# Kernel tuning notes

Hardware: AMD Instinct MI355X
Metric: run time of the kernel (lower is better)

Reference implementation:

```python
import jax, jax.numpy as jnp
import numpy as np

L = 32768          # sequence length (keys/values)
E = 1024           # embed_dim (hardcoded in module via weight slices)
H, D = 8, 128      # num_heads, head_dim (hardcoded via reshape(-1, 8, 128))


def setup_inputs() -> dict:
    key = jax.random.key(0)
    k1, k2, k3, k4, k5 = jax.random.split(key, 5)
    scale = 1.0 / np.sqrt(E)
    return {
        "x": jax.random.normal(k1, (L, E), dtype=jnp.float32),
        "in_proj_weight": jax.random.normal(k2, (3 * E, E), dtype=jnp.float32) * scale,
        "in_proj_bias": jax.random.normal(k3, (3 * E,), dtype=jnp.float32) * 0.02,
        "out_proj_weight": jax.random.normal(k4, (E, E), dtype=jnp.float32) * scale,
        "out_proj_bias": jax.random.normal(k5, (E,), dtype=jnp.float32) * 0.02,
    }


def reference(x, in_proj_weight, in_proj_bias, out_proj_weight, out_proj_bias):
    # Single-query (decode-style) attention: q from first token only.
    q = x[:1] @ in_proj_weight[:E].T + in_proj_bias[:E]              # [1, E]
    k = x @ in_proj_weight[E:2 * E].T + in_proj_bias[E:2 * E]        # [L, E]
    v = x @ in_proj_weight[2 * E:].T + in_proj_bias[2 * E:]          # [L, E]

    q = q.reshape(-1, H, D).transpose(1, 0, 2)                       # [H, 1, D]
    k = k.reshape(-1, H, D).transpose(1, 2, 0)                       # [H, D, L]
    v = v.reshape(-1, H, D).transpose(1, 0, 2)                       # [H, L, D]

    dot = jnp.matmul(q, k) * (1.0 / np.sqrt(D))                      # [H, 1, L]
    attn = jax.nn.softmax(dot, axis=-1)
    out = jnp.matmul(attn, v)                                        # [H, 1, D]

    out = out.transpose(1, 0, 2).reshape(-1, E)                      # [1, E]
    out = out @ out_proj_weight.T + out_proj_bias                    # [1, E]
    return out
```

## Files before the change

kernel.cpp:

```cpp
#include <hip/hip_runtime.h>
#include <math.h>


#define L_SEQ   32768
#define E_DIM   1024
#define NHEAD   8
#define HDIM    128
#define TILE_R  8
#define WAVES_M 8

#define GLD16(gp, lp)                                                   \
  __builtin_amdgcn_global_load_lds(                                     \
      (const __attribute__((address_space(1))) void*)(gp),              \
      (__attribute__((address_space(3))) void*)(lp), 16, 0, 0)

__global__ __launch_bounds__(256) void proj_q(
    const float* __restrict__ W, const float* __restrict__ bias,
    const float* __restrict__ x, float* __restrict__ q)
{
  const int t = threadIdx.x, wave = t >> 6, lane = t & 63;
  const int o = blockIdx.x * 4 + wave;
  const float4* Wr = (const float4*)(W + (size_t)o * E_DIM);
  const float4* xr = (const float4*)x;
  float a = 0.f;
#pragma unroll
  for (int k = 0; k < 4; ++k) {
    float4 wv = Wr[lane + 64 * k];
    float4 xv = xr[lane + 64 * k];
    a += wv.x * xv.x + wv.y * xv.y + wv.z * xv.z + wv.w * xv.w;
  }
#pragma unroll
  for (int m = 1; m < 64; m <<= 1) a += __shfl_xor(a, m, 64);
  if (lane == 0) q[o] = a + bias[o];
}

__global__ __launch_bounds__(256) void make_p(
    const float* __restrict__ W, const float* __restrict__ q,
    float* __restrict__ P_T)
{
  __shared__ __align__(16) float4 ps[8][32];
  const int t  = threadIdx.x;
  const int h  = blockIdx.y;
  const int ec = blockIdx.x;
  const int eg = t & 31;
  const int dg = t >> 5;
  const float* Wb = W + ((size_t)E_DIM + h * HDIM + dg * 16) * E_DIM + ec * 128 + eg * 4;
  const float* qh = q + h * HDIM + dg * 16;
  float4 a = make_float4(0.f, 0.f, 0.f, 0.f);
#pragma unroll
  for (int dd = 0; dd < 16; ++dd) {
    const float qv = qh[dd];
    const float4 wv = *(const float4*)(Wb + (size_t)dd * E_DIM);
    a.x += qv * wv.x; a.y += qv * wv.y; a.z += qv * wv.z; a.w += qv * wv.w;
  }
  ps[dg][eg] = a;
  __syncthreads();
  if (t < 32) {
    float4 s = ps[0][t];
#pragma unroll
    for (int g = 1; g < 8; ++g) {
      const float4 b = ps[g][t];
      s.x += b.x; s.y += b.y; s.z += b.z; s.w += b.w;
    }
    const float sc = 0.08838834764831845f;
    s.x *= sc; s.y *= sc; s.z *= sc; s.w *= sc;
    *(float4*)(P_T + (size_t)h * E_DIM + ec * 128 + t * 4) = s;
  }
}

__global__ __launch_bounds__(512, 2) void attn_fused5(
    const float* __restrict__ x,
    const float* __restrict__ P_T,
    float* __restrict__ partial_z,
    float* __restrict__ partial_sumw,
    int rows_per_blk)
{
  __shared__ __align__(16) float sbuf[2][TILE_R][E_DIM];
  __shared__ float swst[16];

  const int t    = threadIdx.x;
  const int wave = t >> 6;
  const int lane = t & 63;
  const int rh   = wave >> 2;
  const int h0   = (wave & 3) * 2;
  const size_t row0 = (size_t)blockIdx.x * rows_per_blk;
  const int ntiles  = rows_per_blk / TILE_R;

  float4 p0[4], p1[4];
  {
    const float4* P0 = (const float4*)(P_T + (size_t)h0 * E_DIM);
    const float4* P1 = (const float4*)(P_T + (size_t)(h0 + 1) * E_DIM);
#pragma unroll
    for (int k = 0; k < 4; ++k) { p0[k] = P0[64 * k + lane]; p1[k] = P1[64 * k + lane]; }
  }

  float4 z0[4], z1[4];
#pragma unroll
  for (int k = 0; k < 4; ++k) {
    z0[k] = make_float4(0.f, 0.f, 0.f, 0.f);
    z1[k] = make_float4(0.f, 0.f, 0.f, 0.f);
  }
  float sumw0 = 0.f, sumw1 = 0.f;

  {
    const float* g = x + (row0 + wave) * E_DIM + 4 * lane;
#pragma unroll
    for (int k = 0; k < 4; ++k) GLD16(g + k * 256, &sbuf[0][wave][k * 256]);
  }
  __syncthreads();

  for (int tile = 0; tile < ntiles; ++tile) {
    const int buf = tile & 1;

    if (tile + 1 < ntiles) {
      const float* g = x + (row0 + (size_t)(tile + 1) * TILE_R + wave) * E_DIM + 4 * lane;
#pragma unroll
      for (int k = 0; k < 4; ++k) GLD16(g + k * 256, &sbuf[buf ^ 1][wave][k * 256]);
    }

#pragma unroll
    for (int rl = 0; rl < 4; ++rl) {
      const float4* xr4 = (const float4*)&sbuf[buf][rh * 4 + rl][0];
      float4 xr[4];
#pragma unroll
      for (int k = 0; k < 4; ++k) xr[k] = xr4[64 * k + lane];

      float s0 = 0.f, s1 = 0.f;
#pragma unroll
      for (int k = 0; k < 4; ++k) {
        s0 += xr[k].x * p0[k].x + xr[k].y * p0[k].y + xr[k].z * p0[k].z + xr[k].w * p0[k].w;
        s1 += xr[k].x * p1[k].x + xr[k].y * p1[k].y + xr[k].z * p1[k].z + xr[k].w * p1[k].w;
      }

      const bool odd = (lane & 1);
      float keep = odd ? s1 : s0;
      float oth  = odd ? s0 : s1;
      float ts = keep + __shfl_xor(oth, 1, 64);
      ts += __shfl_xor(ts, 2, 64);
      ts += __shfl_xor(ts, 4, 64);
      ts += __shfl_xor(ts, 8, 64);
      ts += __shfl_xor(ts, 16, 64);
      ts += __shfl_xor(ts, 32, 64);
      const float ex = __expf(ts);
      const float ox = __shfl_xor(ex, 1, 64);
      const float w0 = odd ? ox : ex;
      const float w1 = odd ? ex : ox;
      sumw0 += w0; sumw1 += w1;

#pragma unroll
      for (int k = 0; k < 4; ++k) {
        z0[k].x += w0 * xr[k].x; z0[k].y += w0 * xr[k].y;
        z0[k].z += w0 * xr[k].z; z0[k].w += w0 * xr[k].w;
        z1[k].x += w1 * xr[k].x; z1[k].y += w1 * xr[k].y;
        z1[k].z += w1 * xr[k].z; z1[k].w += w1 * xr[k].w;
      }
    }

    __syncthreads();
  }

  float (*zs)[E_DIM] = (float(*)[E_DIM])&sbuf[0][0][0];
  {
    float4* zd0 = (float4*)&zs[2 * wave][0];
    float4* zd1 = (float4*)&zs[2 * wave + 1][0];
#pragma unroll
    for (int k = 0; k < 4; ++k) { zd0[64 * k + lane] = z0[k]; zd1[64 * k + lane] = z1[k]; }
  }
  if (lane == 0) { swst[2 * wave] = sumw0; swst[2 * wave + 1] = sumw1; }
  __syncthreads();

  {
    const float4* zsv = (const float4*)&zs[0][0];
    float4* pzb = (float4*)(partial_z + (size_t)blockIdx.x * (NHEAD * E_DIM));
#pragma unroll
    for (int j = 0; j < 4; ++j) {
      const int idx = t + 512 * j;
      const float4 a = zsv[idx], b = zsv[idx + 2048];
      pzb[idx] = make_float4(a.x + b.x, a.y + b.y, a.z + b.z, a.w + b.w);
    }
  }
  if (t < NHEAD)
    partial_sumw[blockIdx.x * NHEAD + t] = swst[t] + swst[t + 8];
}

__global__ __launch_bounds__(256) void reduce_z(
    const float* __restrict__ partial_z,
    const float* __restrict__ partial_sumw,
    float* __restrict__ zn, int nblk)
{
  __shared__ float red[256];
  __shared__ __align__(16) float swst[4][NHEAD];
  __shared__ float sumw_s[NHEAD];
  const int t = threadIdx.x;
  const int lane = t & 63, wave = t >> 6;

  float sw[NHEAD];
#pragma unroll
  for (int h = 0; h < NHEAD; ++h) sw[h] = 0.f;
  for (int b = t; b < nblk; b += 256) {
    const float4* p = (const float4*)(partial_sumw + (size_t)b * NHEAD);
    float4 a0 = p[0], a1 = p[1];
    sw[0] += a0.x; sw[1] += a0.y; sw[2] += a0.z; sw[3] += a0.w;
    sw[4] += a1.x; sw[5] += a1.y; sw[6] += a1.z; sw[7] += a1.w;
  }
#pragma unroll
  for (int m = 1; m < 64; m <<= 1) {
#pragma unroll
    for (int h = 0; h < NHEAD; ++h) sw[h] += __shfl_xor(sw[h], m, 64);
  }
  if (lane == 0) {
#pragma unroll
    for (int h = 0; h < NHEAD; ++h) swst[wave][h] = sw[h];
  }
  __syncthreads();
  if (t < NHEAD) sumw_s[t] = swst[0][t] + swst[1][t] + swst[2][t] + swst[3][t];

  const int o = blockIdx.x * 32 + (t & 31);
  const int g = t >> 5;
  float a = 0.f;
  for (int b = g; b < nblk; b += 8) a += partial_z[(size_t)b * (NHEAD * E_DIM) + o];
  red[t] = a;
  __syncthreads();
  if (t < 32) {
    float s2 = 0.f;
#pragma unroll
    for (int gg = 0; gg < 8; ++gg) s2 += red[gg * 32 + t];
    const int oo = blockIdx.x * 32 + t;
    zn[oo] = s2 / sumw_s[oo >> 10];
  }
}

__global__ __launch_bounds__(256) void proj_v(
    const float* __restrict__ W, const float* __restrict__ bias,
    const float* __restrict__ zn, float* __restrict__ attn)
{
  const int t = threadIdx.x, wave = t >> 6, lane = t & 63;
  const int o = blockIdx.x * 4 + wave;
  const float4* Wr = (const float4*)(W + ((size_t)2 * E_DIM + o) * E_DIM);
  const float4* zr = (const float4*)(zn + (size_t)(o >> 7) * E_DIM);
  float a = 0.f;
#pragma unroll
  for (int k = 0; k < 4; ++k) {
    float4 wv = Wr[lane + 64 * k];
    float4 zv = zr[lane + 64 * k];
    a += wv.x * zv.x + wv.y * zv.y + wv.z * zv.z + wv.w * zv.w;
  }
#pragma unroll
  for (int m = 1; m < 64; m <<= 1) a += __shfl_xor(a, m, 64);
  if (lane == 0) attn[o] = a + bias[2 * E_DIM + o];
}

__global__ __launch_bounds__(256) void proj_o(
    const float* __restrict__ Wo, const float* __restrict__ bo,
    const float* __restrict__ attn, float* __restrict__ out)
{
  const int t = threadIdx.x, wave = t >> 6, lane = t & 63;
  const int o = blockIdx.x * 4 + wave;
  const float4* Wr = (const float4*)(Wo + (size_t)o * E_DIM);
  const float4* vr = (const float4*)attn;
  float a = 0.f;
#pragma unroll
  for (int k = 0; k < 4; ++k) {
    float4 wv = Wr[lane + 64 * k];
    float4 vv = vr[lane + 64 * k];
    a += wv.x * vv.x + wv.y * vv.y + wv.z * vv.z + wv.w * vv.w;
  }
#pragma unroll
  for (int m = 1; m < 64; m <<= 1) a += __shfl_xor(a, m, 64);
  if (lane == 0) out[o] = a + bo[o];
}

extern "C" void kernel_launch(void* const* d_in, const int* in_sizes, int n_in,
                              void* d_out, int out_size, void* d_ws, size_t ws_size,
                              hipStream_t stream)
{
  const float* x  = (const float*)d_in[0];
  const float* Wi = (const float*)d_in[1];
  const float* bi = (const float*)d_in[2];
  const float* Wo = (const float*)d_in[3];
  const float* bo = (const float*)d_in[4];
  float* out = (float*)d_out;

  char* ws = (char*)d_ws;
  float* q     = (float*)(ws + 0);
  float* P_T   = (float*)(ws + 4096);
  float* zn    = (float*)(ws + 36864);
  float* attn  = (float*)(ws + 69632);
  float* psumw = (float*)(ws + 73728);
  const size_t pz_off = 90112;
  float* pz    = (float*)(ws + pz_off);

  int nblk = 128;
  if (ws_size >= pz_off + (size_t)512 * NHEAD * E_DIM * 4) nblk = 512;
  else if (ws_size >= pz_off + (size_t)256 * NHEAD * E_DIM * 4) nblk = 256;
  const int rows_per_blk = L_SEQ / nblk;

  proj_q     <<<256, 256, 0, stream>>>(Wi, bi, x, q);
  make_p     <<<dim3(8, 8), 256, 0, stream>>>(Wi, q, P_T);
  attn_fused5<<<nblk, 512, 0, stream>>>(x, P_T, pz, psumw, rows_per_blk);
  reduce_z   <<<256, 256, 0, stream>>>(pz, psumw, zn, nblk);
  proj_v     <<<256, 256, 0, stream>>>(Wi, bi, zn, attn);
  proj_o     <<<256, 256, 0, stream>>>(Wo, bo, attn, out);
}
```

Before: 242.6 us.

## Fuse all stages into one persistent kernel with software grid barriers

Replaces the six-kernel launch sequence with a single persistent kernel of 256 blocks that runs q projection, P construction, attention streaming, reduction and both output projections. Stages are separated by an atomic-counter grid barrier, so there is one launch instead of six and no inter-kernel gaps. In exchange, the attention stage uses 256 blocks instead of possibly 512, and the barrier depends on all blocks being co-resident, which could deadlock if they are not. A memset of the barrier is also added each call, and the fallback make_p path is rewritten to use one thread per output.

```diff
diff --git a/kernel.cpp b/kernel.cpp
--- a/kernel.cpp
+++ b/kernel.cpp
@@ -7,12 +7,278 @@
 #define NHEAD   8
 #define HDIM    128
 #define TILE_R  8
-#define WAVES_M 8
+#define NBLK    256
 
 #define GLD16(gp, lp)                                                   \
   __builtin_amdgcn_global_load_lds(                                     \
       (const __attribute__((address_space(1))) void*)(gp),              \
       (__attribute__((address_space(3))) void*)(lp), 16, 0, 0)
+
+__device__ __forceinline__ void grid_barrier(int* bar, int phase)
+{
+  __syncthreads();
+  if (threadIdx.x == 0) {
+    if (__hip_atomic_fetch_add(&bar[0], 1, __ATOMIC_ACQ_REL,
+                               __HIP_MEMORY_SCOPE_AGENT) == NBLK - 1) {
+      __hip_atomic_store(&bar[0], 0, __ATOMIC_RELAXED, __HIP_MEMORY_SCOPE_AGENT);
+      __hip_atomic_store(&bar[1], phase, __ATOMIC_RELEASE, __HIP_MEMORY_SCOPE_AGENT);
+    } else {
+      while (__hip_atomic_load(&bar[1], __ATOMIC_ACQUIRE,
+                               __HIP_MEMORY_SCOPE_AGENT) < phase) {}
+    }
+  }
+  __syncthreads();
+}
+
+__global__ __launch_bounds__(512, 2) void mha_all(
+    const float* __restrict__ x,   const float* __restrict__ Wi,
+    const float* __restrict__ bi,  const float* __restrict__ Wo,
+    const float* __restrict__ bo,  float* __restrict__ out,
+    float* __restrict__ q,   float* __restrict__ P_T,
+    float* __restrict__ zn,  float* __restrict__ attn,
+    float* __restrict__ psumw, float* __restrict__ pz,
+    int* bar)
+{
+  __shared__ __align__(16) float sbuf[2][TILE_R][E_DIM];
+  __shared__ float swst[16];
+  __shared__ __align__(16) float swst4[8][NHEAD];
+  __shared__ float sumw_s[NHEAD];
+
+  const int t    = threadIdx.x;
+  const int wave = t >> 6;
+  const int lane = t & 63;
+  const int bid  = blockIdx.x;
+
+  if (bid < 128) {
+    const int o = bid * 8 + wave;
+    const float4* Wr = (const float4*)(Wi + (size_t)o * E_DIM);
+    const float4* xr = (const float4*)x;
+    float a = 0.f;
+#pragma unroll
+    for (int k = 0; k < 4; ++k) {
+      float4 wv = Wr[lane + 64 * k];
+      float4 xv = xr[lane + 64 * k];
+      a += wv.x * xv.x + wv.y * xv.y + wv.z * xv.z + wv.w * xv.w;
+    }
+#pragma unroll
+    for (int m = 1; m < 64; m <<= 1) a += __shfl_xor(a, m, 64);
+    if (lane == 0) q[o] = a + bi[o];
+  }
+  grid_barrier(bar, 1);
+
+  if (bid < 128) {
+    float4 (*ps)[16] = (float4(*)[16])&sbuf[0][0][0];
+    const int h   = bid >> 4;
+    const int ec2 = bid & 15;
+    const int eg  = t & 15;
+    const int dg  = t >> 4;
+    const float* Wb = Wi + ((size_t)E_DIM + h * HDIM + dg * 4) * E_DIM + ec2 * 64 + eg * 4;
+    const float* qh = q + h * HDIM + dg * 4;
+    float4 a = make_float4(0.f, 0.f, 0.f, 0.f);
+#pragma unroll
+    for (int dd = 0; dd < 4; ++dd) {
+      const float qv = qh[dd];
+      const float4 wv = *(const float4*)(Wb + (size_t)dd * E_DIM);
+      a.x += qv * wv.x; a.y += qv * wv.y; a.z += qv * wv.z; a.w += qv * wv.w;
+    }
+    ps[dg][eg] = a;
+    __syncthreads();
+    if (t < 16) {
+      float4 s = ps[0][t];
+#pragma unroll
+      for (int g = 1; g < 32; ++g) {
+        const float4 b = ps[g][t];
+        s.x += b.x; s.y += b.y; s.z += b.z; s.w += b.w;
+      }
+      const float sc = 0.08838834764831845f;
+      s.x *= sc; s.y *= sc; s.z *= sc; s.w *= sc;
+      *(float4*)(P_T + (size_t)h * E_DIM + ec2 * 64 + t * 4) = s;
+    }
+  }
+  grid_barrier(bar, 2);
+
+  {
+    const int rh = wave >> 2;
+    const int h0 = (wave & 3) * 2;
+    const size_t row0 = (size_t)bid * (L_SEQ / NBLK);
+    const int ntiles  = (L_SEQ / NBLK) / TILE_R;
+
+    float4 p0[4], p1[4];
+    {
+      const float4* P0 = (const float4*)(P_T + (size_t)h0 * E_DIM);
+      const float4* P1 = (const float4*)(P_T + (size_t)(h0 + 1) * E_DIM);
+#pragma unroll
+      for (int k = 0; k < 4; ++k) { p0[k] = P0[64 * k + lane]; p1[k] = P1[64 * k + lane]; }
+    }
+
+    float4 z0[4], z1[4];
+#pragma unroll
+    for (int k = 0; k < 4; ++k) {
+      z0[k] = make_float4(0.f, 0.f, 0.f, 0.f);
+      z1[k] = make_float4(0.f, 0.f, 0.f, 0.f);
+    }
+    float sumw0 = 0.f, sumw1 = 0.f;
+
+    {
+      const float* g = x + (row0 + wave) * E_DIM + 4 * lane;
+#pragma unroll
+      for (int k = 0; k < 4; ++k) GLD16(g + k * 256, &sbuf[0][wave][k * 256]);
+    }
+    __syncthreads();
+
+    for (int tile = 0; tile < ntiles; ++tile) {
+      const int buf = tile & 1;
+
+      if (tile + 1 < ntiles) {
+        const float* g = x + (row0 + (size_t)(tile + 1) * TILE_R + wave) * E_DIM + 4 * lane;
+#pragma unroll
+        for (int k = 0; k < 4; ++k) GLD16(g + k * 256, &sbuf[buf ^ 1][wave][k * 256]);
+      }
+
+#pragma unroll
+      for (int rl = 0; rl < 4; ++rl) {
+        const float4* xr4 = (const float4*)&sbuf[buf][rh * 4 + rl][0];
+        float4 xr[4];
+#pragma unroll
+        for (int k = 0; k < 4; ++k) xr[k] = xr4[64 * k + lane];
+
+        float s0 = 0.f, s1 = 0.f;
+#pragma unroll
+        for (int k = 0; k < 4; ++k) {
+          s0 += xr[k].x * p0[k].x + xr[k].y * p0[k].y + xr[k].z * p0[k].z + xr[k].w * p0[k].w;
+          s1 += xr[k].x * p1[k].x + xr[k].y * p1[k].y + xr[k].z * p1[k].z + xr[k].w * p1[k].w;
+        }
+
+        const bool odd = (lane & 1);
+        float keep = odd ? s1 : s0;
+        float oth  = odd ? s0 : s1;
+        float ts = keep + __shfl_xor(oth, 1, 64);
+        ts += __shfl_xor(ts, 2, 64);
+        ts += __shfl_xor(ts, 4, 64);
+        ts += __shfl_xor(ts, 8, 64);
+        ts += __shfl_xor(ts, 16, 64);
+        ts += __shfl_xor(ts, 32, 64);
+        const float ex = __expf(ts);
+        const float ox = __shfl_xor(ex, 1, 64);
+        const float w0 = odd ? ox : ex;
+        const float w1 = odd ? ex : ox;
+        sumw0 += w0; sumw1 += w1;
+
+#pragma unroll
+        for (int k = 0; k < 4; ++k) {
+          z0[k].x += w0 * xr[k].x; z0[k].y += w0 * xr[k].y;
+          z0[k].z += w0 * xr[k].z; z0[k].w += w0 * xr[k].w;
+          z1[k].x += w1 * xr[k].x; z1[k].y += w1 * xr[k].y;
+          z1[k].z += w1 * xr[k].z; z1[k].w += w1 * xr[k].w;
+        }
+      }
+
+      __syncthreads();
+    }
+
+    float (*zs)[E_DIM] = (float(*)[E_DIM])&sbuf[0][0][0];
+    {
+      float4* zd0 = (float4*)&zs[2 * wave][0];
+      float4* zd1 = (float4*)&zs[2 * wave + 1][0];
+#pragma unroll
+      for (int k = 0; k < 4; ++k) { zd0[64 * k + lane] = z0[k]; zd1[64 * k + lane] = z1[k]; }
+    }
+    if (lane == 0) { swst[2 * wave] = sumw0; swst[2 * wave + 1] = sumw1; }
+    __syncthreads();
+
+    {
+      const float4* zsv = (const float4*)&zs[0][0];
+      float4* pzb = (float4*)(pz + (size_t)bid * (NHEAD * E_DIM));
+#pragma unroll
+      for (int j = 0; j < 4; ++j) {
+        const int idx = t + 512 * j;
+        const float4 a = zsv[idx], b = zsv[idx + 2048];
+        pzb[idx] = make_float4(a.x + b.x, a.y + b.y, a.z + b.z, a.w + b.w);
+      }
+    }
+    if (t < NHEAD)
+      psumw[bid * NHEAD + t] = swst[t] + swst[t + 8];
+  }
+  grid_barrier(bar, 3);
+
+  {
+    float* red = &sbuf[0][0][0];
+    float sw[NHEAD];
+#pragma unroll
+    for (int h = 0; h < NHEAD; ++h) sw[h] = 0.f;
+    for (int b2 = t; b2 < NBLK; b2 += 512) {
+      const float4* p = (const float4*)(psumw + (size_t)b2 * NHEAD);
+      float4 a0 = p[0], a1 = p[1];
+      sw[0] += a0.x; sw[1] += a0.y; sw[2] += a0.z; sw[3] += a0.w;
+      sw[4] += a1.x; sw[5] += a1.y; sw[6] += a1.z; sw[7] += a1.w;
+    }
+#pragma unroll
+    for (int m = 1; m < 64; m <<= 1) {
+#pragma unroll
+      for (int h = 0; h < NHEAD; ++h) sw[h] += __shfl_xor(sw[h], m, 64);
+    }
+    if (lane == 0) {
+#pragma unroll
+      for (int h = 0; h < NHEAD; ++h) swst4[wave][h] = sw[h];
+    }
+    __syncthreads();
+    if (t < NHEAD) {
+      float s = 0.f;
+#pragma unroll
+      for (int wv = 0; wv < 8; ++wv) s += swst4[wv][t];
+      sumw_s[t] = s;
+    }
+
+    const int o = bid * 32 + (t & 31);
+    const int g = t >> 5;
+    float a = 0.f;
+    for (int b2 = g; b2 < NBLK; b2 += 16) a += pz[(size_t)b2 * (NHEAD * E_DIM) + o];
+    red[t] = a;
+    __syncthreads();
+    if (t < 32) {
+      float s2 = 0.f;
+#pragma unroll
+      for (int gg = 0; gg < 16; ++gg) s2 += red[gg * 32 + t];
+      const int oo = bid * 32 + t;
+      zn[oo] = s2 / sumw_s[oo >> 10];
+    }
+  }
+  grid_barrier(bar, 4);
+
+  if (bid < 128) {
+    const int o = bid * 8 + wave;
+    const float4* Wr = (const float4*)(Wi + ((size_t)2 * E_DIM + o) * E_DIM);
+    const float4* zr = (const float4*)(zn + (size_t)(o >> 7) * E_DIM);
+    float a = 0.f;
+#pragma unroll
+    for (int k = 0; k < 4; ++k) {
+      float4 wv = Wr[lane + 64 * k];
+      float4 zv = zr[lane + 64 * k];
+      a += wv.x * zv.x + wv.y * zv.y + wv.z * zv.z + wv.w * zv.w;
+    }
+#pragma unroll
+    for (int m = 1; m < 64; m <<= 1) a += __shfl_xor(a, m, 64);
+    if (lane == 0) attn[o] = a + bi[2 * E_DIM + o];
+  }
+  grid_barrier(bar, 5);
+
+  if (bid < 128) {
+    const int o = bid * 8 + wave;
+    const float4* Wr = (const float4*)(Wo + (size_t)o * E_DIM);
+    const float4* vr = (const float4*)attn;
+    float a = 0.f;
+#pragma unroll
+    for (int k = 0; k < 4; ++k) {
+      float4 wv = Wr[lane + 64 * k];
+      float4 vv = vr[lane + 64 * k];
+      a += wv.x * vv.x + wv.y * vv.y + wv.z * vv.z + wv.w * vv.w;
+    }
+#pragma unroll
+    for (int m = 1; m < 64; m <<= 1) a += __shfl_xor(a, m, 64);
+    if (lane == 0) out[o] = a + bo[o];
+  }
+}
+
 
 __global__ __launch_bounds__(256) void proj_q(
     const float* __restrict__ W, const float* __restrict__ bias,
@@ -34,57 +300,36 @@
   if (lane == 0) q[o] = a + bias[o];
 }
 
-__global__ __launch_bounds__(256) void make_p(
+__global__ __launch_bounds__(128) void make_p(
     const float* __restrict__ W, const float* __restrict__ q,
     float* __restrict__ P_T)
 {
-  __shared__ __align__(16) float4 ps[8][32];
-  const int t  = threadIdx.x;
-  const int h  = blockIdx.y;
-  const int ec = blockIdx.x;
-  const int eg = t & 31;
-  const int dg = t >> 5;
-  const float* Wb = W + ((size_t)E_DIM + h * HDIM + dg * 16) * E_DIM + ec * 128 + eg * 4;
-  const float* qh = q + h * HDIM + dg * 16;
-  float4 a = make_float4(0.f, 0.f, 0.f, 0.f);
-#pragma unroll
-  for (int dd = 0; dd < 16; ++dd) {
-    const float qv = qh[dd];
-    const float4 wv = *(const float4*)(Wb + (size_t)dd * E_DIM);
-    a.x += qv * wv.x; a.y += qv * wv.y; a.z += qv * wv.z; a.w += qv * wv.w;
-  }
-  ps[dg][eg] = a;
-  __syncthreads();
-  if (t < 32) {
-    float4 s = ps[0][t];
-#pragma unroll
-    for (int g = 1; g < 8; ++g) {
-      const float4 b = ps[g][t];
-      s.x += b.x; s.y += b.y; s.z += b.z; s.w += b.w;
-    }
-    const float sc = 0.08838834764831845f;
-    s.x *= sc; s.y *= sc; s.z *= sc; s.w *= sc;
-    *(float4*)(P_T + (size_t)h * E_DIM + ec * 128 + t * 4) = s;
-  }
+  const int h = blockIdx.y;
+  const int e = blockIdx.x * 128 + threadIdx.x;
+  const float* qh = q + h * HDIM;
+  const float* Wb = W + ((size_t)E_DIM + (size_t)h * HDIM) * E_DIM + e;
+  float a0 = 0.f, a1 = 0.f, a2 = 0.f, a3 = 0.f;
+#pragma unroll 4
+  for (int d = 0; d < HDIM; d += 4) {
+    a0 += qh[d + 0] * Wb[(size_t)(d + 0) * E_DIM];
+    a1 += qh[d + 1] * Wb[(size_t)(d + 1) * E_DIM];
+    a2 += qh[d + 2] * Wb[(size_t)(d + 2) * E_DIM];
+    a3 += qh[d + 3] * Wb[(size_t)(d + 3) * E_DIM];
+  }
+  P_T[h * E_DIM + e] = ((a0 + a1) + (a2 + a3)) * 0.08838834764831845f;
 }
 
 __global__ __launch_bounds__(512, 2) void attn_fused5(
-    const float* __restrict__ x,
-    const float* __restrict__ P_T,
-    float* __restrict__ partial_z,
-    float* __restrict__ partial_sumw,
+    const float* __restrict__ x, const float* __restrict__ P_T,
+    float* __restrict__ partial_z, float* __restrict__ partial_sumw,
     int rows_per_blk)
 {
   __shared__ __align__(16) float sbuf[2][TILE_R][E_DIM];
   __shared__ float swst[16];
-
-  const int t    = threadIdx.x;
-  const int wave = t >> 6;
-  const int lane = t & 63;
-  const int rh   = wave >> 2;
-  const int h0   = (wave & 3) * 2;
+  const int t = threadIdx.x, wave = t >> 6, lane = t & 63;
+  const int rh = wave >> 2, h0 = (wave & 3) * 2;
   const size_t row0 = (size_t)blockIdx.x * rows_per_blk;
-  const int ntiles  = rows_per_blk / TILE_R;
+  const int ntiles = rows_per_blk / TILE_R;
 
   float4 p0[4], p1[4];
   {
@@ -93,7 +338,6 @@
 #pragma unroll
     for (int k = 0; k < 4; ++k) { p0[k] = P0[64 * k + lane]; p1[k] = P1[64 * k + lane]; }
   }
-
   float4 z0[4], z1[4];
 #pragma unroll
   for (int k = 0; k < 4; ++k) {
@@ -101,37 +345,31 @@
     z1[k] = make_float4(0.f, 0.f, 0.f, 0.f);
   }
   float sumw0 = 0.f, sumw1 = 0.f;
-
   {
     const float* g = x + (row0 + wave) * E_DIM + 4 * lane;
 #pragma unroll
     for (int k = 0; k < 4; ++k) GLD16(g + k * 256, &sbuf[0][wave][k * 256]);
   }
   __syncthreads();
-
   for (int tile = 0; tile < ntiles; ++tile) {
     const int buf = tile & 1;
-
     if (tile + 1 < ntiles) {
       const float* g = x + (row0 + (size_t)(tile + 1) * TILE_R + wave) * E_DIM + 4 * lane;
 #pragma unroll
       for (int k = 0; k < 4; ++k) GLD16(g + k * 256, &sbuf[buf ^ 1][wave][k * 256]);
     }
-
 #pragma unroll
     for (int rl = 0; rl < 4; ++rl) {
       const float4* xr4 = (const float4*)&sbuf[buf][rh * 4 + rl][0];
       float4 xr[4];
 #pragma unroll
       for (int k = 0; k < 4; ++k) xr[k] = xr4[64 * k + lane];
-
       float s0 = 0.f, s1 = 0.f;
 #pragma unroll
       for (int k = 0; k < 4; ++k) {
         s0 += xr[k].x * p0[k].x + xr[k].y * p0[k].y + xr[k].z * p0[k].z + xr[k].w * p0[k].w;
         s1 += xr[k].x * p1[k].x + xr[k].y * p1[k].y + xr[k].z * p1[k].z + xr[k].w * p1[k].w;
       }
-
       const bool odd = (lane & 1);
       float keep = odd ? s1 : s0;
       float oth  = odd ? s0 : s1;
@@ -146,7 +384,6 @@
       const float w0 = odd ? ox : ex;
       const float w1 = odd ? ex : ox;
       sumw0 += w0; sumw1 += w1;
-
 #pragma unroll
       for (int k = 0; k < 4; ++k) {
         z0[k].x += w0 * xr[k].x; z0[k].y += w0 * xr[k].y;
@@ -155,10 +392,8 @@
         z1[k].z += w1 * xr[k].z; z1[k].w += w1 * xr[k].w;
       }
     }
-
     __syncthreads();
   }
-
   float (*zs)[E_DIM] = (float(*)[E_DIM])&sbuf[0][0][0];
   {
     float4* zd0 = (float4*)&zs[2 * wave][0];
@@ -168,7 +403,6 @@
   }
   if (lane == 0) { swst[2 * wave] = sumw0; swst[2 * wave + 1] = sumw1; }
   __syncthreads();
-
   {
     const float4* zsv = (const float4*)&zs[0][0];
     float4* pzb = (float4*)(partial_z + (size_t)blockIdx.x * (NHEAD * E_DIM));
@@ -184,8 +418,7 @@
 }
 
 __global__ __launch_bounds__(256) void reduce_z(
-    const float* __restrict__ partial_z,
-    const float* __restrict__ partial_sumw,
+    const float* __restrict__ partial_z, const float* __restrict__ partial_sumw,
     float* __restrict__ zn, int nblk)
 {
   __shared__ float red[256];
@@ -193,7 +426,6 @@
   __shared__ float sumw_s[NHEAD];
   const int t = threadIdx.x;
   const int lane = t & 63, wave = t >> 6;
-
   float sw[NHEAD];
 #pragma unroll
   for (int h = 0; h < NHEAD; ++h) sw[h] = 0.f;
@@ -214,7 +446,6 @@
   }
   __syncthreads();
   if (t < NHEAD) sumw_s[t] = swst[0][t] + swst[1][t] + swst[2][t] + swst[3][t];
-
   const int o = blockIdx.x * 32 + (t & 31);
   const int g = t >> 5;
   float a = 0.f;
@@ -287,8 +518,17 @@
   float* zn    = (float*)(ws + 36864);
   float* attn  = (float*)(ws + 69632);
   float* psumw = (float*)(ws + 73728);
+  int*   bar   = (int*)  (ws + 81920);
   const size_t pz_off = 90112;
   float* pz    = (float*)(ws + pz_off);
+
+  const size_t need_coop = pz_off + (size_t)NBLK * NHEAD * E_DIM * 4;
+  if (ws_size >= need_coop) {
+    hipMemsetAsync(bar, 0, 64, stream);
+    mha_all<<<NBLK, 512, 0, stream>>>(x, Wi, bi, Wo, bo, out,
+                                      q, P_T, zn, attn, psumw, pz, bar);
+    return;
+  }
 
   int nblk = 128;
   if (ws_size >= pz_off + (size_t)512 * NHEAD * E_DIM * 4) nblk = 512;
@@ -296,7 +536,7 @@
   const int rows_per_blk = L_SEQ / nblk;
 
   proj_q     <<<256, 256, 0, stream>>>(Wi, bi, x, q);
-  make_p     <<<dim3(8, 8), 256, 0, stream>>>(Wi, q, P_T);
+  make_p     <<<dim3(8, 8), 128, 0, stream>>>(Wi, q, P_T);
   attn_fused5<<<nblk, 512, 0, stream>>>(x, P_T, pz, psumw, rows_per_blk);
   reduce_z   <<<256, 256, 0, stream>>>(pz, psumw, zn, nblk);
   proj_v     <<<256, 256, 0, stream>>>(Wi, bi, zn, attn);
```

Measured after the change: 351.0 us. 44.7% more time.
